# Optimization experiments

Hardware: AMD Instinct MI355X
Metric: run time of the kernel (lower is better)

Reference implementation:

```python
import jax, jax.numpy as jnp
import numpy as np

N = 50000          # nodes
E = 1600000        # edges (before self-loops)
DIN = 128
HEADS = (8, 8, 4)
FEATS = (16, 16, 16)
NEG_SLOPE = 0.2


def setup_inputs() -> dict:
    key = jax.random.key(0)
    ks = jax.random.split(key, 2 + 4 * 3)
    inp = {
        "X": jax.random.normal(ks[0], (N, DIN), dtype=jnp.float32),
        "A": jax.random.randint(ks[1], (2, E), 0, N, dtype=jnp.int32),
    }
    in_dims = [DIN, HEADS[0] * FEATS[0], HEADS[1] * FEATS[1]]
    k = 2
    for i, (h, f) in enumerate(zip(HEADS, FEATS)):
        din = in_dims[i]
        concat = i + 1 < len(HEADS)
        inp[f"W{i+1}"] = jax.random.normal(ks[k], (din, h * f), dtype=jnp.float32) / np.float32(np.sqrt(din)); k += 1
        inp[f"as{i+1}"] = jax.random.normal(ks[k], (h, f), dtype=jnp.float32) * 0.1; k += 1
        inp[f"ad{i+1}"] = jax.random.normal(ks[k], (h, f), dtype=jnp.float32) * 0.1; k += 1
        inp[f"b{i+1}"] = jnp.zeros((h * f if concat else f,), dtype=jnp.float32); k += 1
    return inp


def _gat_conv(x, src, dst, W, a_src, a_dst, b, concat):
    # PyG-style GATConv (eval mode, self-loops already in src/dst)
    H, F = a_src.shape
    h = (x @ W).reshape(-1, H, F)                     # [N, H, F]
    e = jax.nn.leaky_relu((h * a_src).sum(-1)[src] + (h * a_dst).sum(-1)[dst], NEG_SLOPE)  # [Etot, H]
    m = jax.ops.segment_max(e, dst, num_segments=N)   # segment softmax over dst neighborhoods
    ex = jnp.exp(e - m[dst])
    s = jax.ops.segment_sum(ex, dst, num_segments=N)
    alpha = ex / (s[dst] + 1e-16)                     # [Etot, H]
    out = jax.ops.segment_sum(h[src] * alpha[:, :, None], dst, num_segments=N)  # [N, H, F]
    out = out.reshape(N, H * F) if concat else out.mean(axis=1)
    return out + b


def reference(X, A, W1, as1, ad1, b1, W2, as2, ad2, b2, W3, as3, ad3, b3):
    loops = jnp.arange(N, dtype=A.dtype)              # GATConv default add_self_loops=True
    src = jnp.concatenate([A[0], loops])
    dst = jnp.concatenate([A[1], loops])
    x = jax.nn.relu(_gat_conv(X, src, dst, W1, as1, ad1, b1, True))
    x = jax.nn.relu(_gat_conv(x, src, dst, W2, as2, ad2, b2, True))
    return _gat_conv(x, src, dst, W3, as3, ad3, b3, False)
```

## Files before the change

kernel.cpp:

```cpp
#include <hip/hip_runtime.h>
#include <hip/hip_bf16.h>

#define NN 50000
#define EE 1600000
#define DIN 128

#define BKT_SHIFT 6
#define NB ((NN + 63) >> 6)
#define BSLACK 2688
#define CHUNK 4096

typedef _Float16 half_t;
typedef __attribute__((ext_vector_type(2))) _Float16 half2_t;
typedef __attribute__((ext_vector_type(4))) _Float16 half4_t;
typedef __attribute__((ext_vector_type(8))) _Float16 half8_t;
typedef __attribute__((ext_vector_type(4))) float float4_t;

__device__ __forceinline__ void split_write(half_t* __restrict__ bh, half_t* __restrict__ bl,
                                            int idx, float v) {
    half_t h = (half_t)v;
    bh[idx] = h;
    bl[idx] = (half_t)(v - (float)h);
}

__device__ __forceinline__ void build_bt(const float* __restrict__ W,
                                         const float* __restrict__ as,
                                         const float* __restrict__ ad,
                                         half_t* __restrict__ Bh, half_t* __restrict__ Bl,
                                         int elem, int NCOL, int H) {
    int r = elem >> 7, k = elem & 127;
    float v;
    if (r < NCOL) {
        v = W[k * NCOL + r];
    } else {
        int j = r - NCOL;
        v = 0.f;
        if (j < 8) {
            if (j < H) {
                float s = 0.f;
#pragma unroll
                for (int f = 0; f < 16; ++f) s += W[k * NCOL + j * 16 + f] * as[j * 16 + f];
                v = s;
            }
        } else {
            int hh = j - 8;
            if (hh < H) {
                float s = 0.f;
#pragma unroll
                for (int f = 0; f < 16; ++f) s += W[k * NCOL + hh * 16 + f] * ad[hh * 16 + f];
                v = s;
            }
        }
    }
    split_write(Bh, Bl, r * 128 + k, v);
}

#define T1 (144 * 128)
#define T3 (80 * 128)
__global__ __launch_bounds__(256) void prep_kernel(
    const float* __restrict__ W1, const float* __restrict__ W2, const float* __restrict__ W3,
    const float* __restrict__ as1, const float* __restrict__ ad1,
    const float* __restrict__ as2, const float* __restrict__ ad2,
    const float* __restrict__ as3, const float* __restrict__ ad3,
    half_t* __restrict__ B1h, half_t* __restrict__ B1l,
    half_t* __restrict__ B2h, half_t* __restrict__ B2l,
    half_t* __restrict__ B3h, half_t* __restrict__ B3l,
    int* __restrict__ gcursor) {
    int id = blockIdx.x * 256 + threadIdx.x;
    if (id < T1) {
        build_bt(W1, as1, ad1, B1h, B1l, id, 128, 8);
    } else if (id < 2 * T1) {
        build_bt(W2, as2, ad2, B2h, B2l, id - T1, 128, 8);
    } else if (id < 2 * T1 + T3) {
        build_bt(W3, as3, ad3, B3h, B3l, id - 2 * T1, 64, 4);
    } else {
        int i = id - (2 * T1 + T3);
        if (i < NB) gcursor[i] = 0;
    }
}

__global__ __launch_bounds__(256) void bin_kernel(const int* __restrict__ A,
                                                  int* __restrict__ gcursor,
                                                  int* __restrict__ binned, int e, int n) {
    __shared__ int lcount[NB];
    __shared__ int lbase[NB];
    int chunk0 = blockIdx.x * CHUNK;
    int cend = chunk0 + CHUNK;
    if (cend > e + n) cend = e + n;
    for (int i = threadIdx.x; i < NB; i += 256) lcount[i] = 0;
    __syncthreads();
    int sreg[16], dreg[16];
#pragma unroll
    for (int l = 0; l < 16; ++l) {
        int i = chunk0 + l * 256 + threadIdx.x;
        if (i < cend) {
            if (i < e) { sreg[l] = A[i]; dreg[l] = A[e + i]; }
            else       { sreg[l] = dreg[l] = i - e; }
            atomicAdd(&lcount[dreg[l] >> BKT_SHIFT], 1);
        } else {
            dreg[l] = -1;
        }
    }
    __syncthreads();
    for (int b = threadIdx.x; b < NB; b += 256) {
        int c = lcount[b];
        lbase[b] = c ? atomicAdd(&gcursor[b], c) : 0;
        lcount[b] = 0;
    }
    __syncthreads();
#pragma unroll
    for (int l = 0; l < 16; ++l) {
        if (dreg[l] >= 0) {
            int bkt = dreg[l] >> BKT_SHIFT;
            int pos = lbase[bkt] + atomicAdd(&lcount[bkt], 1);
            if (pos < BSLACK)
                binned[(size_t)bkt * BSLACK + pos] = (sreg[l] << 6) | (dreg[l] & 63);
        }
    }
}

__global__ __launch_bounds__(256) void fine_scatter(const int* __restrict__ binned,
                                                    const int* __restrict__ gcursor,
                                                    int* __restrict__ begE,
                                                    int* __restrict__ endE,
                                                    int* __restrict__ csr) {
    __shared__ int lc[64];
    __shared__ int scur[64];
    int b = blockIdx.x;
    int node0 = b << BKT_SHIFT;
    int cnt = gcursor[b];
    if (cnt > BSLACK) cnt = BSLACK;
    const int* bp = binned + (size_t)b * BSLACK;
    if (threadIdx.x < 64) lc[threadIdx.x] = 0;
    __syncthreads();
    for (int j = threadIdx.x; j < cnt; j += 256) atomicAdd(&lc[bp[j] & 63], 1);
    __syncthreads();
    if (threadIdx.x < 64) {
        int lane = threadIdx.x;
        int c = lc[lane];
        int v = c;
#pragma unroll
        for (int off = 1; off < 64; off <<= 1) {
            int u = __shfl_up(v, off, 64);
            if (lane >= off) v += u;
        }
        int begin = b * BSLACK + v - c;
        scur[lane] = begin;
        int node = node0 + lane;
        if (node < NN) {
            begE[node] = begin;
            endE[node] = begin + c;
        }
    }
    __syncthreads();
    for (int j = threadIdx.x; j < cnt; j += 256) {
        int v = bp[j];
        int pos = atomicAdd(&scur[v & 63], 1);
        csr[pos] = v >> 6;
    }
}

template <int NTC, int H, bool A32>
__global__ __launch_bounds__(256) void gemm_mfma(
    const float* __restrict__ X32,
    const half_t* __restrict__ Ah, const half_t* __restrict__ Al,
    const half_t* __restrict__ Bth, const half_t* __restrict__ Btl,
    half_t* __restrict__ C16, float* __restrict__ ss, float* __restrict__ ds, int M) {
    constexpr int NCOL = NTC * 16;
    __shared__ __align__(16) half_t cs[4][16][NCOL + 8];
    int tid = threadIdx.x;
    int w = tid >> 6, lane = tid & 63;
    int m = lane & 15, q = lane >> 4;
    int row0 = blockIdx.x * 64 + w * 16;

    int ar = row0 + m;
    if (ar >= M) ar = M - 1;
    half8_t ahf[4], alf[4];
    if constexpr (A32) {
        const float* px = X32 + (size_t)ar * 128 + q * 8;
#pragma unroll
        for (int k0 = 0; k0 < 4; ++k0) {
            float4 u0 = *(const float4*)(px + k0 * 32);
            float4 u1 = *(const float4*)(px + k0 * 32 + 4);
            float uv[8] = {u0.x, u0.y, u0.z, u0.w, u1.x, u1.y, u1.z, u1.w};
#pragma unroll
            for (int j = 0; j < 8; ++j) {
                half_t h = (half_t)uv[j];
                ahf[k0][j] = h;
                alf[k0][j] = (half_t)(uv[j] - (float)h);
            }
        }
    } else {
        const half_t* pa = Ah + (size_t)ar * 128 + q * 8;
        const half_t* pl = Al + (size_t)ar * 128 + q * 8;
#pragma unroll
        for (int k0 = 0; k0 < 4; ++k0) {
            ahf[k0] = *(const half8_t*)(pa + k0 * 32);
            alf[k0] = *(const half8_t*)(pl + k0 * 32);
        }
    }

    float4_t acc[NTC + 1];
#pragma unroll
    for (int nt = 0; nt <= NTC; ++nt) {
        acc[nt][0] = 0.f; acc[nt][1] = 0.f; acc[nt][2] = 0.f; acc[nt][3] = 0.f;
    }

#pragma unroll
    for (int nt = 0; nt <= NTC; ++nt) {
        const half_t* pbh = Bth + (size_t)(nt * 16 + m) * 128 + q * 8;
        const half_t* pbl = Btl + (size_t)(nt * 16 + m) * 128 + q * 8;
        half8_t bh[4], bl[4];
#pragma unroll
        for (int k0 = 0; k0 < 4; ++k0) {
            bh[k0] = *(const half8_t*)(pbh + k0 * 32);
            bl[k0] = *(const half8_t*)(pbl + k0 * 32);
        }
#pragma unroll
        for (int k0 = 0; k0 < 4; ++k0) {
            acc[nt] = __builtin_amdgcn_mfma_f32_16x16x32_f16(ahf[k0], bh[k0], acc[nt], 0, 0, 0);
            acc[nt] = __builtin_amdgcn_mfma_f32_16x16x32_f16(ahf[k0], bl[k0], acc[nt], 0, 0, 0);
            acc[nt] = __builtin_amdgcn_mfma_f32_16x16x32_f16(alf[k0], bh[k0], acc[nt], 0, 0, 0);
        }
    }

#pragma unroll
    for (int r = 0; r < 4; ++r) {
        int grow = row0 + q * 4 + r;
        if (grow < M) {
            float v = acc[NTC][r];
            if (m < H) ss[(size_t)grow * H + m] = v;
            else if (m >= 8 && m < 8 + H) ds[(size_t)grow * H + (m - 8)] = v;
        }
    }

#pragma unroll
    for (int nt = 0; nt < NTC; ++nt)
#pragma unroll
        for (int r = 0; r < 4; ++r)
            cs[w][q * 4 + r][nt * 16 + m] = (half_t)acc[nt][r];
    constexpr int LPR = NCOL / 8;
    constexpr int RPP = 64 / LPR;
    constexpr int NP = 16 / RPP;
    int rid = lane / LPR, cid = lane % LPR;
#pragma unroll
    for (int p = 0; p < NP; ++p) {
        int r = p * RPP + rid;
        int grow = row0 + r;
        half8_t v = *(const half8_t*)&cs[w][r][cid * 8];
        if (grow < M) *(half8_t*)(C16 + (size_t)grow * NCOL + cid * 8) = v;
    }
}

template <int H, int F, bool MEAN, bool RELU>
__global__ __launch_bounds__(256) void aggregate_qw(
    const half_t* __restrict__ h, const float* __restrict__ ss, const float* __restrict__ dsc_arr,
    const int* __restrict__ csr, const int* __restrict__ begE, const int* __restrict__ endE,
    const float* __restrict__ bias, half_t* __restrict__ outh, half_t* __restrict__ outl,
    float* __restrict__ out, int n) {
    constexpr int HF = H * F;
    constexpr int FPL = HF / 16;
    int wave = blockIdx.x * (blockDim.x >> 6) + (threadIdx.x >> 6);
    int lane = threadIdx.x & 63;
    if (wave >= n) return;
    int q = lane >> 4, ql = lane & 15;
    int hf = ql * FPL;
    int hh = hf / F;
    float dsc = dsc_arr[wave * H + hh];
    int begin = begE[wave], end = endE[wave];

    float ssum = 0.f;
    float acc[FPL];
#pragma unroll
    for (int k = 0; k < FPL; ++k) acc[k] = 0.f;

    int j = begin + q;
    for (; j + 12 < end; j += 16) {
        int s0 = csr[j], s1 = csr[j + 4], s2 = csr[j + 8], s3 = csr[j + 12];
        float e0 = ss[s0 * H + hh], e1 = ss[s1 * H + hh];
        float e2 = ss[s2 * H + hh], e3 = ss[s3 * H + hh];
        const half_t* p0 = h + (size_t)s0 * HF + hf;
        const half_t* p1 = h + (size_t)s1 * HF + hf;
        const half_t* p2 = h + (size_t)s2 * HF + hf;
        const half_t* p3 = h + (size_t)s3 * HF + hf;
        e0 += dsc; e0 = (e0 > 0.f) ? e0 : 0.2f * e0;
        e1 += dsc; e1 = (e1 > 0.f) ? e1 : 0.2f * e1;
        e2 += dsc; e2 = (e2 > 0.f) ? e2 : 0.2f * e2;
        e3 += dsc; e3 = (e3 > 0.f) ? e3 : 0.2f * e3;
        float x0 = __expf(e0), x1 = __expf(e1), x2 = __expf(e2), x3 = __expf(e3);
        ssum += (x0 + x1) + (x2 + x3);
        if constexpr (FPL == 8) {
            half8_t t0 = *(const half8_t*)p0, t1 = *(const half8_t*)p1;
            half8_t t2 = *(const half8_t*)p2, t3 = *(const half8_t*)p3;
#pragma unroll
            for (int k = 0; k < 8; ++k) {
                acc[k] = fmaf(x0, (float)t0[k], acc[k]);
                acc[k] = fmaf(x1, (float)t1[k], acc[k]);
                acc[k] = fmaf(x2, (float)t2[k], acc[k]);
                acc[k] = fmaf(x3, (float)t3[k], acc[k]);
            }
        } else {
            half4_t t0 = *(const half4_t*)p0, t1 = *(const half4_t*)p1;
            half4_t t2 = *(const half4_t*)p2, t3 = *(const half4_t*)p3;
#pragma unroll
            for (int k = 0; k < 4; ++k) {
                acc[k] = fmaf(x0, (float)t0[k], acc[k]);
                acc[k] = fmaf(x1, (float)t1[k], acc[k]);
                acc[k] = fmaf(x2, (float)t2[k], acc[k]);
                acc[k] = fmaf(x3, (float)t3[k], acc[k]);
            }
        }
    }
    for (; j + 4 < end; j += 8) {
        int s0 = csr[j], s1 = csr[j + 4];
        float e0 = ss[s0 * H + hh], e1 = ss[s1 * H + hh];
        const half_t* p0 = h + (size_t)s0 * HF + hf;
        const half_t* p1 = h + (size_t)s1 * HF + hf;
        e0 += dsc; e0 = (e0 > 0.f) ? e0 : 0.2f * e0;
        e1 += dsc; e1 = (e1 > 0.f) ? e1 : 0.2f * e1;
        float x0 = __expf(e0), x1 = __expf(e1);
        ssum += x0 + x1;
        if constexpr (FPL == 8) {
            half8_t t0 = *(const half8_t*)p0, t1 = *(const half8_t*)p1;
#pragma unroll
            for (int k = 0; k < 8; ++k) {
                acc[k] = fmaf(x0, (float)t0[k], acc[k]);
                acc[k] = fmaf(x1, (float)t1[k], acc[k]);
            }
        } else {
            half4_t t0 = *(const half4_t*)p0, t1 = *(const half4_t*)p1;
#pragma unroll
            for (int k = 0; k < 4; ++k) {
                acc[k] = fmaf(x0, (float)t0[k], acc[k]);
                acc[k] = fmaf(x1, (float)t1[k], acc[k]);
            }
        }
    }
    for (; j < end; j += 4) {
        int s = csr[j];
        float e = ss[s * H + hh] + dsc;
        e = (e > 0.f) ? e : 0.2f * e;
        float x = __expf(e);
        ssum += x;
        const half_t* hp = h + (size_t)s * HF + hf;
        if constexpr (FPL == 8) {
            half8_t t = *(const half8_t*)hp;
#pragma unroll
            for (int k = 0; k < 8; ++k) acc[k] = fmaf(x, (float)t[k], acc[k]);
        } else {
            half4_t t = *(const half4_t*)hp;
#pragma unroll
            for (int k = 0; k < 4; ++k) acc[k] = fmaf(x, (float)t[k], acc[k]);
        }
    }

    ssum += __shfl_xor(ssum, 16, 64);
    ssum += __shfl_xor(ssum, 32, 64);
#pragma unroll
    for (int k = 0; k < FPL; ++k) {
        acc[k] += __shfl_xor(acc[k], 16, 64);
        acc[k] += __shfl_xor(acc[k], 32, 64);
    }

    float inv = 1.f / (ssum + 1e-16f);
    if constexpr (!MEAN) {
        if (lane < 32) {
            int k0 = (lane >> 4) * 4;
            int f = (lane & 15) * FPL + k0;
            float v[4];
#pragma unroll
            for (int i = 0; i < 4; ++i) {
                v[i] = acc[k0 + i] * inv + bias[f + i];
                if (RELU) v[i] = fmaxf(v[i], 0.f);
            }
            half4_t hh4, ll4;
#pragma unroll
            for (int i = 0; i < 4; ++i) {
                hh4[i] = (half_t)v[i];
                ll4[i] = (half_t)(v[i] - (float)hh4[i]);
            }
            *(half4_t*)(outh + (size_t)wave * HF + f) = hh4;
            *(half4_t*)(outl + (size_t)wave * HF + f) = ll4;
        }
    } else {
        float val[FPL];
#pragma unroll
        for (int k = 0; k < FPL; ++k) {
            val[k] = acc[k] * inv;
            val[k] += __shfl_xor(val[k], 4, 64);
            val[k] += __shfl_xor(val[k], 8, 64);
        }
        if (lane < 4) {
            float v0 = val[0] * 0.25f + bias[lane * 4 + 0];
            float v1 = val[1] * 0.25f + bias[lane * 4 + 1];
            float v2 = val[2] * 0.25f + bias[lane * 4 + 2];
            float v3 = val[3] * 0.25f + bias[lane * 4 + 3];
            *(float4*)(out + (size_t)wave * F + lane * 4) = make_float4(v0, v1, v2, v3);
        }
    }
}

extern "C" void kernel_launch(void* const* d_in, const int* in_sizes, int n_in,
                              void* d_out, int out_size, void* d_ws, size_t ws_size,
                              hipStream_t stream) {
    const float* X  = (const float*)d_in[0];
    const int*   A  = (const int*)d_in[1];
    const float* W1 = (const float*)d_in[2];
    const float* as1 = (const float*)d_in[3];
    const float* ad1 = (const float*)d_in[4];
    const float* b1  = (const float*)d_in[5];
    const float* W2 = (const float*)d_in[6];
    const float* as2 = (const float*)d_in[7];
    const float* ad2 = (const float*)d_in[8];
    const float* b2  = (const float*)d_in[9];
    const float* W3 = (const float*)d_in[10];
    const float* as3 = (const float*)d_in[11];
    const float* ad3 = (const float*)d_in[12];
    const float* b3  = (const float*)d_in[13];

    const int N = NN, E = EE;
    const int Etot = E + N;

    char* p = (char*)d_ws;
    auto take = [&](size_t bytes) {
        char* r = p;
        p += (bytes + 255) & ~(size_t)255;
        return (void*)r;
    };
    half_t* C16   = (half_t*)take((size_t)N * 128 * 2);
    half_t* Ph    = (half_t*)take((size_t)N * 128 * 2);
    half_t* Pl    = (half_t*)take((size_t)N * 128 * 2);
    float* ssb    = (float*)take((size_t)N * 8 * 4);
    float* dsb    = (float*)take((size_t)N * 8 * 4);
    int* begE     = (int*)take((size_t)N * 4);
    int* endE     = (int*)take((size_t)N * 4);
    int* gcursor  = (int*)take((size_t)NB * 4);
    int* csr      = (int*)take((size_t)NB * BSLACK * 4);
    half_t* B1h   = (half_t*)take(144 * 128 * 2);
    half_t* B1l   = (half_t*)take(144 * 128 * 2);
    half_t* B2h   = (half_t*)take(144 * 128 * 2);
    half_t* B2l   = (half_t*)take(144 * 128 * 2);
    half_t* B3h   = (half_t*)take(80 * 128 * 2);
    half_t* B3l   = (half_t*)take(80 * 128 * 2);
    int* binned   = (int*)Ph;

    const int prepTotal = 2 * T1 + T3 + NB;
    prep_kernel<<<(prepTotal + 255) / 256, 256, 0, stream>>>(
        W1, W2, W3, as1, ad1, as2, ad2, as3, ad3,
        B1h, B1l, B2h, B2l, B3h, B3l, gcursor);
    bin_kernel<<<(Etot + CHUNK - 1) / CHUNK, 256, 0, stream>>>(A, gcursor, binned, E, N);
    fine_scatter<<<NB, 256, 0, stream>>>(binned, gcursor, begE, endE, csr);

    const int gemmRows = (N + 63) / 64;
    const int aggBlocks = (N + 3) / 4;

    gemm_mfma<8, 8, true><<<gemmRows, 256, 0, stream>>>(X, nullptr, nullptr,
                                                        B1h, B1l, C16, ssb, dsb, N);
    aggregate_qw<8, 16, false, true>
        <<<aggBlocks, 256, 0, stream>>>(C16, ssb, dsb, csr, begE, endE, b1, Ph, Pl, nullptr, N);

    gemm_mfma<8, 8, false><<<gemmRows, 256, 0, stream>>>(nullptr, Ph, Pl,
                                                         B2h, B2l, C16, ssb, dsb, N);
    aggregate_qw<8, 16, false, true>
        <<<aggBlocks, 256, 0, stream>>>(C16, ssb, dsb, csr, begE, endE, b2, Ph, Pl, nullptr, N);

    gemm_mfma<4, 4, false><<<gemmRows, 256, 0, stream>>>(nullptr, Ph, Pl,
                                                         B3h, B3l, C16, ssb, dsb, N);
    aggregate_qw<4, 16, true, false>
        <<<aggBlocks, 256, 0, stream>>>(C16, ssb, dsb, csr, begE, endE, b3, nullptr, nullptr,
                                        (float*)d_out, N);
}
```

Measured before the change: 398.0 us.

## Use 256-node destination buckets and split aggregation into two half launches

Destination bucketing widens from 64 to 256 nodes per bucket, with slack resized to match. The fine scatter now uses a 256-wide shared-memory scan and 8-bit local indices. This cuts the bucket count, so the bin kernel touches fewer global cursors and fine_scatter launches fewer, larger blocks. Each aggregation launch is also split into two launches over node halves, which adds launch overhead and has no clear benefit beyond possibly better cache locality.

```diff
diff --git a/kernel.cpp b/kernel.cpp
--- a/kernel.cpp
+++ b/kernel.cpp
@@ -5,9 +5,9 @@
 #define EE 1600000
 #define DIN 128
 
-#define BKT_SHIFT 6
-#define NB ((NN + 63) >> 6)
-#define BSLACK 2688
+#define BKT_SHIFT 8
+#define NB ((NN + 255) >> 8)
+#define BSLACK 9472
 #define CHUNK 4096
 
 typedef _Float16 half_t;
@@ -114,7 +114,7 @@
             int bkt = dreg[l] >> BKT_SHIFT;
             int pos = lbase[bkt] + atomicAdd(&lcount[bkt], 1);
             if (pos < BSLACK)
-                binned[(size_t)bkt * BSLACK + pos] = (sreg[l] << 6) | (dreg[l] & 63);
+                binned[(size_t)bkt * BSLACK + pos] = (sreg[l] << 8) | (dreg[l] & 255);
         }
     }
 }
@@ -124,29 +124,31 @@
                                                     int* __restrict__ begE,
                                                     int* __restrict__ endE,
                                                     int* __restrict__ csr) {
-    __shared__ int lc[64];
-    __shared__ int scur[64];
+    __shared__ int lc[256];
+    __shared__ int scur[256];
+    __shared__ int sscan[256];
     int b = blockIdx.x;
     int node0 = b << BKT_SHIFT;
     int cnt = gcursor[b];
     if (cnt > BSLACK) cnt = BSLACK;
     const int* bp = binned + (size_t)b * BSLACK;
-    if (threadIdx.x < 64) lc[threadIdx.x] = 0;
-    __syncthreads();
-    for (int j = threadIdx.x; j < cnt; j += 256) atomicAdd(&lc[bp[j] & 63], 1);
-    __syncthreads();
-    if (threadIdx.x < 64) {
-        int lane = threadIdx.x;
-        int c = lc[lane];
-        int v = c;
-#pragma unroll
-        for (int off = 1; off < 64; off <<= 1) {
-            int u = __shfl_up(v, off, 64);
-            if (lane >= off) v += u;
-        }
-        int begin = b * BSLACK + v - c;
-        scur[lane] = begin;
-        int node = node0 + lane;
+    lc[threadIdx.x] = 0;
+    __syncthreads();
+    for (int j = threadIdx.x; j < cnt; j += 256) atomicAdd(&lc[bp[j] & 255], 1);
+    __syncthreads();
+    int c = lc[threadIdx.x];
+    sscan[threadIdx.x] = c;
+    __syncthreads();
+    for (int off = 1; off < 256; off <<= 1) {
+        int u = (threadIdx.x >= (unsigned)off) ? sscan[threadIdx.x - off] : 0;
+        __syncthreads();
+        sscan[threadIdx.x] += u;
+        __syncthreads();
+    }
+    {
+        int begin = b * BSLACK + sscan[threadIdx.x] - c;
+        scur[threadIdx.x] = begin;
+        int node = node0 + threadIdx.x;
         if (node < NN) {
             begE[node] = begin;
             endE[node] = begin + c;
@@ -155,8 +157,8 @@
     __syncthreads();
     for (int j = threadIdx.x; j < cnt; j += 256) {
         int v = bp[j];
-        int pos = atomicAdd(&scur[v & 63], 1);
-        csr[pos] = v >> 6;
+        int pos = atomicAdd(&scur[v & 255], 1);
+        csr[pos] = v >> 8;
     }
 }
 
@@ -257,12 +259,12 @@
     const half_t* __restrict__ h, const float* __restrict__ ss, const float* __restrict__ dsc_arr,
     const int* __restrict__ csr, const int* __restrict__ begE, const int* __restrict__ endE,
     const float* __restrict__ bias, half_t* __restrict__ outh, half_t* __restrict__ outl,
-    float* __restrict__ out, int n) {
+    float* __restrict__ out, int n0, int n1) {
     constexpr int HF = H * F;
     constexpr int FPL = HF / 16;
-    int wave = blockIdx.x * (blockDim.x >> 6) + (threadIdx.x >> 6);
+    int wave = n0 + blockIdx.x * (blockDim.x >> 6) + (threadIdx.x >> 6);
     int lane = threadIdx.x & 63;
-    if (wave >= n) return;
+    if (wave >= n1) return;
     int q = lane >> 4, ql = lane & 15;
     int hf = ql * FPL;
     int hh = hf / F;
@@ -452,21 +454,27 @@
     fine_scatter<<<NB, 256, 0, stream>>>(binned, gcursor, begE, endE, csr);
 
     const int gemmRows = (N + 63) / 64;
-    const int aggBlocks = (N + 3) / 4;
+    const int NH = 25000;
+    const int halfBlocks = (NH + 3) / 4;
 
     gemm_mfma<8, 8, true><<<gemmRows, 256, 0, stream>>>(X, nullptr, nullptr,
                                                         B1h, B1l, C16, ssb, dsb, N);
-    aggregate_qw<8, 16, false, true>
-        <<<aggBlocks, 256, 0, stream>>>(C16, ssb, dsb, csr, begE, endE, b1, Ph, Pl, nullptr, N);
+    aggregate_qw<8, 16, false, true><<<halfBlocks, 256, 0, stream>>>(
+        C16, ssb, dsb, csr, begE, endE, b1, Ph, Pl, nullptr, 0, NH);
+    aggregate_qw<8, 16, false, true><<<halfBlocks, 256, 0, stream>>>(
+        C16, ssb, dsb, csr, begE, endE, b1, Ph, Pl, nullptr, NH, N);
 
     gemm_mfma<8, 8, false><<<gemmRows, 256, 0, stream>>>(nullptr, Ph, Pl,
                                                          B2h, B2l, C16, ssb, dsb, N);
-    aggregate_qw<8, 16, false, true>
-        <<<aggBlocks, 256, 0, stream>>>(C16, ssb, dsb, csr, begE, endE, b2, Ph, Pl, nullptr, N);
+    aggregate_qw<8, 16, false, true><<<halfBlocks, 256, 0, stream>>>(
+        C16, ssb, dsb, csr, begE, endE, b2, Ph, Pl, nullptr, 0, NH);
+    aggregate_qw<8, 16, false, true><<<halfBlocks, 256, 0, stream>>>(
+        C16, ssb, dsb, csr, begE, endE, b2, Ph, Pl, nullptr, NH, N);
 
     gemm_mfma<4, 4, false><<<gemmRows, 256, 0, stream>>>(nullptr, Ph, Pl,
                                                          B3h, B3l, C16, ssb, dsb, N);
-    aggregate_qw<4, 16, true, false>
-        <<<aggBlocks, 256, 0, stream>>>(C16, ssb, dsb, csr, begE, endE, b3, nullptr, nullptr,
-                                        (float*)d_out, N);
-}
+    aggregate_qw<4, 16, true, false><<<halfBlocks, 256, 0, stream>>>(
+        C16, ssb, dsb, csr, begE, endE, b3, nullptr, nullptr, (float*)d_out, 0, NH);
+    aggregate_qw<4, 16, true, false><<<halfBlocks, 256, 0, stream>>>(
+        C16, ssb, dsb, csr, begE, endE, b3, nullptr, nullptr, (float*)d_out, NH, N);
+}
```

Measured after the change: 418.6 us. +5.2%, slower.
